# Kernel optimization log

Hardware: AMD Instinct MI355X
Metric: run time of the kernel (lower is better)

Reference implementation:

```python
import jax, jax.numpy as jnp
import numpy as np

B = 32768
P = 32  # max_poles == max_zeros
NC = P + 1  # count classes 0..32
BIG = 1e30

POLE_COUNT_W = 5.0
ZERO_COUNT_W = 5.0
POLE_VALUE_W = 1.0
ZERO_VALUE_W = 1.0


def setup_inputs() -> dict:
    key = jax.random.key(0)
    ks = jax.random.split(key, 8)
    return {
        "pole_count_logits": jax.random.normal(ks[0], (B, NC), jnp.float32),
        "zero_count_logits": jax.random.normal(ks[1], (B, NC), jnp.float32),
        "poles_all": jax.random.normal(ks[2], (B, P, 2), jnp.float32),
        "zeros_all": jax.random.normal(ks[3], (B, P, 2), jnp.float32),
        "target_poles_pad": jax.random.normal(ks[4], (B, P, 2), jnp.float32),
        "target_zeros_pad": jax.random.normal(ks[5], (B, P, 2), jnp.float32),
        "target_num_poles": jax.random.randint(ks[6], (B,), 0, NC, jnp.int32),
        "target_num_zeros": jax.random.randint(ks[7], (B,), 0, NC, jnp.int32),
    }


def _cross_entropy(logits, targets):
    logp = jax.nn.log_softmax(logits, axis=-1)
    nll = -jnp.take_along_axis(logp, targets[:, None].astype(jnp.int32), axis=1)[:, 0]
    return jnp.mean(nll)


def _masked_chamfer(pred, tgt, n_pred, n_tgt):
    """Vectorized variable-length chamfer. pred/tgt: [B,P,2], counts: [B]."""
    ar = jnp.arange(pred.shape[1])
    pm = ar[None, :] < n_pred[:, None]  # [B,P] valid pred mask
    tm = ar[None, :] < n_tgt[:, None]   # [B,P] valid target mask
    diff = pred[:, :, None, :] - tgt[:, None, :, :]  # [B,P,T,2]
    d = jnp.sum(diff * diff, axis=-1)                # [B,P,T] |z_p - z_t|^2
    min_p2t = jnp.min(jnp.where(tm[:, None, :], d, BIG), axis=2)  # [B,P]
    mean_p2t = jnp.sum(jnp.where(pm, min_p2t, 0.0), axis=1) / jnp.maximum(n_pred, 1).astype(pred.dtype)
    min_t2p = jnp.min(jnp.where(pm[:, :, None], d, BIG), axis=1)  # [B,T]
    mean_t2p = jnp.sum(jnp.where(tm, min_t2p, 0.0), axis=1) / jnp.maximum(n_tgt, 1).astype(pred.dtype)
    both = mean_p2t + mean_t2p
    sum_tgt_sq = jnp.sum(jnp.where(tm[:, :, None], tgt * tgt, 0.0), axis=(1, 2))
    sum_pred_sq = jnp.sum(jnp.where(pm[:, :, None], pred * pred, 0.0), axis=(1, 2))
    p0 = n_pred == 0
    t0 = n_tgt == 0
    out = jnp.where(p0 & t0, 0.0,
          jnp.where(p0, sum_tgt_sq,
          jnp.where(t0, sum_pred_sq, both)))
    return out  # [B]


def reference(pole_count_logits, zero_count_logits, poles_all, zeros_all,
              target_poles_pad, target_zeros_pad, target_num_poles, target_num_zeros):
    loss_pole_count = _cross_entropy(pole_count_logits, target_num_poles)
    loss_zero_count = _cross_entropy(zero_count_logits, target_num_zeros)

    pred_pole_counts = jnp.argmax(pole_count_logits, axis=-1).astype(jnp.int32)
    pred_zero_counts = jnp.argmax(zero_count_logits, axis=-1).astype(jnp.int32)

    pole_losses = _masked_chamfer(poles_all, target_poles_pad, pred_pole_counts, target_num_poles)
    zero_losses = _masked_chamfer(zeros_all, target_zeros_pad, pred_zero_counts, target_num_zeros)
    loss_pole_value = jnp.mean(pole_losses)
    loss_zero_value = jnp.mean(zero_losses)

    total_loss = (POLE_COUNT_W * loss_pole_count + ZERO_COUNT_W * loss_zero_count
                  + POLE_VALUE_W * loss_pole_value + ZERO_VALUE_W * loss_zero_value)
    return total_loss
```

## Files before the change

### kernel.cpp

```cpp
#include <hip/hip_runtime.h>
#include <float.h>

#define NCNT 33
#define NPTS 32

template<int CTRL, bool BC>
__device__ __forceinline__ int dpp_i(int old, int v) {
    return __builtin_amdgcn_update_dpp(old, v, CTRL, 0xF, 0xF, BC);
}

__device__ __forceinline__ float wave_sum63(float v) {
    v += __int_as_float(dpp_i<0x111, true>(0, __float_as_int(v)));
    v += __int_as_float(dpp_i<0x112, true>(0, __float_as_int(v)));
    v += __int_as_float(dpp_i<0x114, true>(0, __float_as_int(v)));
    v += __int_as_float(dpp_i<0x118, true>(0, __float_as_int(v)));
    v += __int_as_float(dpp_i<0x142, true>(0, __float_as_int(v)));
    v += __int_as_float(dpp_i<0x143, true>(0, __float_as_int(v)));
    return __int_as_float(__builtin_amdgcn_readlane(__float_as_int(v), 63));
}

__device__ __forceinline__ float wave_max63(float v) {
#define MX_STEP(C)                                                                    \
    {                                                                                 \
        int o = dpp_i<C, false>(__float_as_int(v), __float_as_int(v));                \
        v = fmaxf(v, __int_as_float(o));                                              \
    }
    MX_STEP(0x111) MX_STEP(0x112) MX_STEP(0x114) MX_STEP(0x118) MX_STEP(0x142) MX_STEP(0x143)
#undef MX_STEP
    return __int_as_float(__builtin_amdgcn_readlane(__float_as_int(v), 63));
}

__global__ __launch_bounds__(256) void vltf_kernel(
    const float* __restrict__ pole_logits, const float* __restrict__ zero_logits,
    const float* __restrict__ poles_all,   const float* __restrict__ zeros_all,
    const float* __restrict__ tpoles,      const float* __restrict__ tzeros,
    const int* __restrict__ tnum_p,        const int* __restrict__ tnum_z,
    float* __restrict__ partials)
{
    __shared__ __align__(16) float lds[4][136];
    __shared__ float acc[4];

    const int wid  = __builtin_amdgcn_readfirstlane(threadIdx.x >> 6);
    const int lane = threadIdx.x & 63;
    const int unit = blockIdx.x * 4 + wid;
    const int row  = unit >> 1;
    const int part = unit & 1;

    const float* logits = part ? zero_logits : pole_logits;
    const float* predp  = part ? zeros_all   : poles_all;
    const float* tgtp   = part ? tzeros      : tpoles;
    const int*   tnum   = part ? tnum_z      : tnum_p;

    float x = (lane < NCNT) ? logits[row * NCNT + lane] : -FLT_MAX;
    float vmax = wave_max63(x);
    unsigned long long bm = __ballot(lane < NCNT && x == vmax);
    const int np = (int)__builtin_ctzll(bm);
    float e = (lane < NCNT) ? __expf(x - vmax) : 0.f;
    float sume = wave_sum63(e);
    const int nt = tnum[row];
    float xt = __int_as_float(__builtin_amdgcn_readlane(__float_as_int(x), nt));
    float nll = vmax + __logf(sume) - xt;

    const bool isPred = lane < 32;
    const int  idx    = lane & 31;
    const float2* ownArr = (const float2*)(isPred ? predp : tgtp);
    const float2  Pt     = ownArr[row * NPTS + idx];
    const int  nown = isPred ? np : nt;
    const bool vown = idx < nown;
    float* myl = &lds[wid][0];
    {
        float2* wr = (float2*)(myl + (isPred ? 68 : 0));
        wr[idx] = make_float2(vown ? Pt.x : 1e15f, vown ? Pt.y : 1e15f);
    }
    __syncthreads();

    const float4* ov = (const float4*)(myl + (isPred ? 0 : 68));
    float m = FLT_MAX;
#pragma unroll
    for (int i = 0; i < 16; ++i) {
        float4 o = ov[i];
        float dx0 = Pt.x - o.x, dy0 = Pt.y - o.y;
        float dx1 = Pt.x - o.z, dy1 = Pt.y - o.w;
        float d0 = dx0 * dx0 + dy0 * dy0;
        float d1 = dx1 * dx1 + dy1 * dy1;
        m = fminf(fminf(m, d0), d1);
    }

    float T;
    if (np > 0 && nt > 0) {
        T = vown ? (m / (float)nown) : 0.f;
    } else if (np == 0 && nt == 0) {
        T = 0.f;
    } else if (np == 0) {
        T = (!isPred && vown) ? (Pt.x * Pt.x + Pt.y * Pt.y) : 0.f;
    } else {
        T = (isPred && vown) ? (Pt.x * Pt.x + Pt.y * Pt.y) : 0.f;
    }
    float cham = wave_sum63(T);

    float unitv = 5.f * nll + cham;
    if (lane == 0) acc[wid] = unitv;
    __syncthreads();
    if (threadIdx.x == 0)
        partials[blockIdx.x] = acc[0] + acc[1] + acc[2] + acc[3];
}

__global__ __launch_bounds__(256) void vltf_finalize(
    const float4* __restrict__ p4, int n4, float invB, float* __restrict__ out)
{
    float s = 0.f;
    for (int i = threadIdx.x; i < n4; i += 256) {
        float4 v = p4[i];
        s += (v.x + v.y) + (v.z + v.w);
    }
    s = wave_sum63(s);
    __shared__ float sh[4];
    if ((threadIdx.x & 63) == 0) sh[threadIdx.x >> 6] = s;
    __syncthreads();
    if (threadIdx.x == 0) out[0] = (sh[0] + sh[1] + sh[2] + sh[3]) * invB;
}

extern "C" void kernel_launch(void* const* d_in, const int* in_sizes, int n_in,
                              void* d_out, int out_size, void* d_ws, size_t ws_size,
                              hipStream_t stream) {
    const float* pole_logits = (const float*)d_in[0];
    const float* zero_logits = (const float*)d_in[1];
    const float* poles_all   = (const float*)d_in[2];
    const float* zeros_all   = (const float*)d_in[3];
    const float* tpoles      = (const float*)d_in[4];
    const float* tzeros      = (const float*)d_in[5];
    const int*   tnp         = (const int*)d_in[6];
    const int*   tnz         = (const int*)d_in[7];

    const int B      = in_sizes[6];
    const int units  = 2 * B;
    const int blocks = units / 4;

    float* partials = (float*)d_ws;

    vltf_kernel<<<blocks, 256, 0, stream>>>(pole_logits, zero_logits,
                                            poles_all, zeros_all,
                                            tpoles, tzeros, tnp, tnz, partials);
    vltf_finalize<<<1, 256, 0, stream>>>((const float4*)partials, blocks / 4,
                                         1.0f / (float)B, (float*)d_out);
}
```

Measured before the change: 113.7 us.

## Expand squared distance algebraically with packed FMA and drop block-level reduction

Rewrites the chamfer distance as |p|^2 - 2p·t + |t|^2. Each point's -2x, -2y and squared norm are stored in LDS, and the inner loop runs as packed two-wide FMAs followed by mins. The per-block LDS accumulation and second barrier are removed: each wave writes its own partial directly, and the finalize kernel is widened to 1024 threads to sum the larger partials array. The expansion can lose some floating-point accuracy through cancellation, and the finalize step now reads four times as many partials.

```diff
diff --git a/kernel.cpp b/kernel.cpp
--- a/kernel.cpp
+++ b/kernel.cpp
@@ -3,6 +3,10 @@
 
 #define NCNT 33
 #define NPTS 32
+
+typedef float f32x2 __attribute__((ext_vector_type(2)));
+
+__device__ __forceinline__ f32x2 mk2(float a, float b) { f32x2 r; r.x = a; r.y = b; return r; }
 
 template<int CTRL, bool BC>
 __device__ __forceinline__ int dpp_i(int old, int v) {
@@ -37,8 +41,7 @@
     const int* __restrict__ tnum_p,        const int* __restrict__ tnum_z,
     float* __restrict__ partials)
 {
-    __shared__ __align__(16) float lds[4][136];
-    __shared__ float acc[4];
+    __shared__ __align__(16) float lds[4][192];
 
     const int wid  = __builtin_amdgcn_readfirstlane(threadIdx.x >> 6);
     const int lane = threadIdx.x & 63;
@@ -67,57 +70,67 @@
     const float2  Pt     = ownArr[row * NPTS + idx];
     const int  nown = isPred ? np : nt;
     const bool vown = idx < nown;
+    const float sreal = fmaf(Pt.x, Pt.x, Pt.y * Pt.y);
+
     float* myl = &lds[wid][0];
-    {
-        float2* wr = (float2*)(myl + (isPred ? 68 : 0));
-        wr[idx] = make_float2(vown ? Pt.x : 1e15f, vown ? Pt.y : 1e15f);
-    }
+    const int wbase = isPred ? 96 : 0;
+    const int uvpos = wbase + ((idx >> 1) << 2) + (idx & 1);
+    myl[uvpos]          = vown ? -2.f * Pt.x : 0.f;
+    myl[uvpos + 2]      = vown ? -2.f * Pt.y : 0.f;
+    myl[wbase + 64 + idx] = vown ? sreal : 1e30f;
     __syncthreads();
 
-    const float4* ov = (const float4*)(myl + (isPred ? 0 : 68));
+    const int rbase = isPred ? 0 : 96;
+    const float4* UVo = (const float4*)(myl + rbase);
+    const float4* So  = (const float4*)(myl + rbase + 64);
+    const f32x2 Pxv = mk2(Pt.x, Pt.x);
+    const f32x2 Pyv = mk2(Pt.y, Pt.y);
     float m = FLT_MAX;
 #pragma unroll
-    for (int i = 0; i < 16; ++i) {
-        float4 o = ov[i];
-        float dx0 = Pt.x - o.x, dy0 = Pt.y - o.y;
-        float dx1 = Pt.x - o.z, dy1 = Pt.y - o.w;
-        float d0 = dx0 * dx0 + dy0 * dy0;
-        float d1 = dx1 * dx1 + dy1 * dy1;
-        m = fminf(fminf(m, d0), d1);
+    for (int i = 0; i < 8; ++i) {
+        float4 uv0 = UVo[2 * i], uv1 = UVo[2 * i + 1];
+        float4 s4  = So[i];
+        f32x2 val0 = Pyv * mk2(uv0.z, uv0.w) + mk2(s4.x, s4.y);
+        val0       = Pxv * mk2(uv0.x, uv0.y) + val0;
+        f32x2 val1 = Pyv * mk2(uv1.z, uv1.w) + mk2(s4.z, s4.w);
+        val1       = Pxv * mk2(uv1.x, uv1.y) + val1;
+        m = fminf(m, fminf(val0.x, val0.y));
+        m = fminf(m, fminf(val1.x, val1.y));
     }
 
     float T;
     if (np > 0 && nt > 0) {
-        T = vown ? (m / (float)nown) : 0.f;
+        T = vown ? (m + sreal) / (float)nown : 0.f;
     } else if (np == 0 && nt == 0) {
         T = 0.f;
     } else if (np == 0) {
-        T = (!isPred && vown) ? (Pt.x * Pt.x + Pt.y * Pt.y) : 0.f;
+        T = (!isPred && vown) ? sreal : 0.f;
     } else {
-        T = (isPred && vown) ? (Pt.x * Pt.x + Pt.y * Pt.y) : 0.f;
+        T = (isPred && vown) ? sreal : 0.f;
     }
     float cham = wave_sum63(T);
 
-    float unitv = 5.f * nll + cham;
-    if (lane == 0) acc[wid] = unitv;
-    __syncthreads();
-    if (threadIdx.x == 0)
-        partials[blockIdx.x] = acc[0] + acc[1] + acc[2] + acc[3];
+    if (lane == 0) partials[unit] = 5.f * nll + cham;
 }
 
-__global__ __launch_bounds__(256) void vltf_finalize(
+__global__ __launch_bounds__(1024) void vltf_finalize(
     const float4* __restrict__ p4, int n4, float invB, float* __restrict__ out)
 {
     float s = 0.f;
-    for (int i = threadIdx.x; i < n4; i += 256) {
+    for (int i = threadIdx.x; i < n4; i += 1024) {
         float4 v = p4[i];
         s += (v.x + v.y) + (v.z + v.w);
     }
     s = wave_sum63(s);
-    __shared__ float sh[4];
+    __shared__ float sh[16];
     if ((threadIdx.x & 63) == 0) sh[threadIdx.x >> 6] = s;
     __syncthreads();
-    if (threadIdx.x == 0) out[0] = (sh[0] + sh[1] + sh[2] + sh[3]) * invB;
+    if (threadIdx.x == 0) {
+        float t = 0.f;
+#pragma unroll
+        for (int i = 0; i < 16; ++i) t += sh[i];
+        out[0] = t * invB;
+    }
 }
 
 extern "C" void kernel_launch(void* const* d_in, const int* in_sizes, int n_in,
@@ -141,6 +154,6 @@
     vltf_kernel<<<blocks, 256, 0, stream>>>(pole_logits, zero_logits,
                                             poles_all, zeros_all,
                                             tpoles, tzeros, tnp, tnz, partials);
-    vltf_finalize<<<1, 256, 0, stream>>>((const float4*)partials, blocks / 4,
-                                         1.0f / (float)B, (float*)d_out);
+    vltf_finalize<<<1, 1024, 0, stream>>>((const float4*)partials, units / 4,
+                                          1.0f / (float)B, (float*)d_out);
 }
```

After: 110.2 us. 1.03x faster.
